# Performance work log

Hardware: AMD Instinct MI355X
Metric: run time of the kernel (lower is better)

Reference implementation:

```python
import jax, jax.numpy as jnp
import numpy as np

B, N, D, K = 4, 2048, 64, 256


def setup_inputs() -> dict:
    key = jax.random.key(0)
    k1, k2 = jax.random.split(key)
    x = jax.random.normal(k1, (B, N, D), dtype=jnp.float32)
    # glorot_uniform over last two dims (D, K)
    limit = np.sqrt(6.0 / (D + K)).astype(np.float32)
    table = jax.random.uniform(k2, (1, 1, D, K), minval=-limit, maxval=limit, dtype=jnp.float32)
    scale = jnp.ones((1, 1, 1), dtype=jnp.float32)
    return {"x": x, "table": table, "scale": scale}


def reference(x, table, scale):
    # diff: [B, N, D, K] = table[1,1,D,K] - x[B,N,D,1]
    diff = table - x[..., None]
    # out: [B, N, K]
    out = jnp.abs(scale) * jnp.sum(diff * diff, axis=-2)
    return out
```

## Files before the change

### kernel.cpp

```cpp
#include <hip/hip_runtime.h>


#define TD_D    64
#define TD_K    256
#define TD_ROWS 8

__global__ void TableDistance_5669356831001_kernel(
    const float* __restrict__ x,
    const float* __restrict__ table,
    const float* __restrict__ scale,
    float* __restrict__ out)
{
    const int k    = threadIdx.x;
    const int row0 = blockIdx.x * TD_ROWS;

    __shared__ float xs[TD_ROWS][TD_D];
    __shared__ float x2s[TD_ROWS];

    const float* xbase = x + (size_t)row0 * TD_D;
    float* xs_flat = &xs[0][0];
    #pragma unroll
    for (int i = 0; i < (TD_ROWS * TD_D) / 256; ++i) {
        xs_flat[threadIdx.x + i * 256] = xbase[threadIdx.x + i * 256];
    }
    __syncthreads();

    if (threadIdx.x < TD_ROWS) {
        float s = 0.f;
        #pragma unroll
        for (int d = 0; d < TD_D; ++d) {
            float v = xs[threadIdx.x][d];
            s = fmaf(v, v, s);
        }
        x2s[threadIdx.x] = s;
    }
    __syncthreads();

    float acc[TD_ROWS];
    #pragma unroll
    for (int r = 0; r < TD_ROWS; ++r) acc[r] = 0.f;
    float t2 = 0.f;

    #pragma unroll
    for (int d = 0; d < TD_D; ++d) {
        float t = table[d * TD_K + k];
        t2 = fmaf(t, t, t2);
        #pragma unroll
        for (int r = 0; r < TD_ROWS; ++r) {
            acc[r] = fmaf(t, xs[r][d], acc[r]);
        }
    }

    const float s = fabsf(scale[0]);
    float* obase = out + (size_t)row0 * TD_K + k;
    #pragma unroll
    for (int r = 0; r < TD_ROWS; ++r) {
        obase[r * TD_K] = s * (t2 + x2s[r] - 2.0f * acc[r]);
    }
}

extern "C" void kernel_launch(void* const* d_in, const int* in_sizes, int n_in,
                              void* d_out, int out_size, void* d_ws, size_t ws_size,
                              hipStream_t stream) {
    const float* x     = (const float*)d_in[0];
    const float* table = (const float*)d_in[1];
    const float* scale = (const float*)d_in[2];
    float* out = (float*)d_out;

    const int nrows = 4 * 2048;
    const int grid  = nrows / TD_ROWS;
    TableDistance_5669356831001_kernel<<<grid, TD_K, 0, stream>>>(x, table, scale, out);
}
```

Measured before the change: 12.39 us.

## Use single-wave blocks with float4 table columns and shuffle-based row norms

Each block becomes one 64-lane wavefront handling 4 rows, and each lane now computes 4 adjacent output columns using float4 loads of the table and float4 stores. Row squared norms are computed with wave shuffles instead of a serial loop by 8 threads, which removes one __syncthreads. The grid doubles to 2048 blocks, and each block reads the full 64 KB table for only 4 rows, so total table traffic through cache doubles.

```diff
diff --git a/kernel.cpp b/kernel.cpp
--- a/kernel.cpp
+++ b/kernel.cpp
@@ -1,9 +1,11 @@
 #include <hip/hip_runtime.h>
 
 
-#define TD_D    64
-#define TD_K    256
-#define TD_ROWS 8
+#define TD_D 64
+#define TD_K 256
+#define TD_R 4
+
+typedef float f4 __attribute__((ext_vector_type(4)));
 
 __global__ void TableDistance_5669356831001_kernel(
     const float* __restrict__ x,
@@ -11,51 +13,51 @@
     const float* __restrict__ scale,
     float* __restrict__ out)
 {
-    const int k    = threadIdx.x;
-    const int row0 = blockIdx.x * TD_ROWS;
+    const int lane = threadIdx.x;
+    const int row0 = blockIdx.x * TD_R;
 
-    __shared__ float xs[TD_ROWS][TD_D];
-    __shared__ float x2s[TD_ROWS];
+    __shared__ f4 xs[TD_R][TD_D / 4];
 
-    const float* xbase = x + (size_t)row0 * TD_D;
-    float* xs_flat = &xs[0][0];
+    const int sr = lane >> 4, sc = lane & 15;
+    f4 xv = *(const f4*)&x[(size_t)(row0 + sr) * TD_D + sc * 4];
+    xs[sr][sc] = xv;
+
+    float px = xv.x * xv.x + xv.y * xv.y + xv.z * xv.z + xv.w * xv.w;
+    px += __shfl_xor(px, 1);
+    px += __shfl_xor(px, 2);
+    px += __shfl_xor(px, 4);
+    px += __shfl_xor(px, 8);
+    float x2[TD_R];
     #pragma unroll
-    for (int i = 0; i < (TD_ROWS * TD_D) / 256; ++i) {
-        xs_flat[threadIdx.x + i * 256] = xbase[threadIdx.x + i * 256];
-    }
+    for (int r = 0; r < TD_R; ++r) x2[r] = __shfl(px, r * 16);
+
     __syncthreads();
 
-    if (threadIdx.x < TD_ROWS) {
-        float s = 0.f;
-        #pragma unroll
-        for (int d = 0; d < TD_D; ++d) {
-            float v = xs[threadIdx.x][d];
-            s = fmaf(v, v, s);
-        }
-        x2s[threadIdx.x] = s;
-    }
-    __syncthreads();
-
-    float acc[TD_ROWS];
+    const f4* tb = (const f4*)table;
+    f4 acc[TD_R];
     #pragma unroll
-    for (int r = 0; r < TD_ROWS; ++r) acc[r] = 0.f;
-    float t2 = 0.f;
+    for (int r = 0; r < TD_R; ++r) acc[r] = (f4){0.f, 0.f, 0.f, 0.f};
+    f4 t2 = {0.f, 0.f, 0.f, 0.f};
 
     #pragma unroll
-    for (int d = 0; d < TD_D; ++d) {
-        float t = table[d * TD_K + k];
-        t2 = fmaf(t, t, t2);
+    for (int dc = 0; dc < TD_D / 4; ++dc) {
+        f4 t0 = tb[(dc * 4 + 0) * 64 + lane];
+        f4 t1 = tb[(dc * 4 + 1) * 64 + lane];
+        f4 t2v = tb[(dc * 4 + 2) * 64 + lane];
+        f4 t3 = tb[(dc * 4 + 3) * 64 + lane];
+        t2 += t0 * t0 + t1 * t1 + t2v * t2v + t3 * t3;
         #pragma unroll
-        for (int r = 0; r < TD_ROWS; ++r) {
-            acc[r] = fmaf(t, xs[r][d], acc[r]);
+        for (int r = 0; r < TD_R; ++r) {
+            f4 xc = xs[r][dc];
+            acc[r] += t0 * xc.x + t1 * xc.y + t2v * xc.z + t3 * xc.w;
         }
     }
 
     const float s = fabsf(scale[0]);
-    float* obase = out + (size_t)row0 * TD_K + k;
     #pragma unroll
-    for (int r = 0; r < TD_ROWS; ++r) {
-        obase[r * TD_K] = s * (t2 + x2s[r] - 2.0f * acc[r]);
+    for (int r = 0; r < TD_R; ++r) {
+        f4 res = s * (t2 + x2[r] - 2.0f * acc[r]);
+        *(f4*)&out[(size_t)(row0 + r) * TD_K + lane * 4] = res;
     }
 }
 
@@ -68,6 +70,6 @@
     float* out = (float*)d_out;
 
     const int nrows = 4 * 2048;
-    const int grid  = nrows / TD_ROWS;
-    TableDistance_5669356831001_kernel<<<grid, TD_K, 0, stream>>>(x, table, scale, out);
+    const int grid  = nrows / TD_R;
+    TableDistance_5669356831001_kernel<<<grid, 64, 0, stream>>>(x, table, scale, out);
 }
```

Result: slower. 13.12 us (+5.8%).
